# Performance work log

Hardware: AMD Instinct MI355X
Metric: run time of the kernel (lower is better)

Reference implementation:

```python
import jax, jax.numpy as jnp
import numpy as np

N_NODES = 50000
N_EDGES = 800000
IN_DIM = 128
HID = 128
OUT_DIM = 128
N_LAYERS = 6
NUM_GRAPHS = 128


def setup_inputs() -> dict:
    key = jax.random.key(0)
    ks = jax.random.split(key, 16)
    s = 0.05
    inp = {
        "x": jax.random.normal(ks[0], (N_NODES, IN_DIM), jnp.float32),
        "edge_index": jax.random.randint(ks[1], (2, N_EDGES), 0, N_NODES, jnp.int64 if jax.config.jax_enable_x64 else jnp.int32).astype(jnp.int32),
        "batch": jnp.sort(jax.random.randint(ks[2], (N_NODES,), 0, NUM_GRAPHS).astype(jnp.int32)),
        # pre linear
        "pre_w": jax.random.normal(ks[3], (IN_DIM, HID), jnp.float32) * s,
        "pre_b": jnp.zeros((HID,), jnp.float32),
        # GIN mlp per layer: Linear(H,H) -> ReLU -> Linear(H,H)
        "conv_w1": jax.random.normal(ks[4], (N_LAYERS, HID, HID), jnp.float32) * s,
        "conv_b1": jnp.zeros((N_LAYERS, HID), jnp.float32),
        "conv_w2": jax.random.normal(ks[5], (N_LAYERS, HID, HID), jnp.float32) * s,
        "conv_b2": jnp.zeros((N_LAYERS, HID), jnp.float32),
        # post MLP: Linear(7H, H) -> ReLU -> Linear(H, out)
        "post_w1": jax.random.normal(ks[6], (HID * (N_LAYERS + 1), HID), jnp.float32) * s,
        "post_b1": jnp.zeros((HID,), jnp.float32),
        "post_w2": jax.random.normal(ks[7], (HID, OUT_DIM), jnp.float32) * s,
        "post_b2": jnp.zeros((OUT_DIM,), jnp.float32),
    }
    return inp


def reference(x, edge_index, batch, pre_w, pre_b, conv_w1, conv_b1, conv_w2, conv_b2,
              post_w1, post_b1, post_w2, post_b2):
    src, dst = edge_index[0], edge_index[1]
    # pre linear
    h = x @ pre_w + pre_b  # [N, H]
    emb_list = [h]
    xres = h
    for i in range(N_LAYERS):
        # GINConv (eps=0): agg_j x_j over in-edges, then (1+eps)*x + agg -> MLP
        msg = h[src]  # [E, H] gather
        agg = jax.ops.segment_sum(msg, dst, num_segments=N_NODES)  # scatter-add
        z = h + agg
        z = jax.nn.relu(z @ conv_w1[i] + conv_b1[i]) @ conv_w2[i] + conv_b2[i]
        if i & 1:
            z = z + xres
            xres = z
        h = jax.nn.relu(z)
        emb_list.append(h)
    emb = jnp.concatenate(emb_list, axis=1)  # [N, (L+1)*H]
    # global add pool over graphs
    pooled = jax.ops.segment_sum(emb, batch, num_segments=NUM_GRAPHS)  # [G, (L+1)*H]
    out = jax.nn.relu(pooled @ post_w1 + post_b1) @ post_w2 + post_b2  # [G, OUT]
    return out
```

## Files before the change

### kernel.cpp

```cpp
#include <hip/hip_runtime.h>
#include <hip/hip_bf16.h>

#define HID 128

using bf16x8 = __attribute__((ext_vector_type(8))) short;
using f32x4  = __attribute__((ext_vector_type(4))) float;

__device__ inline float bf2f(unsigned int u16) {
    union { float f; unsigned int i; } v; v.i = u16 << 16; return v.f;
}
__device__ inline unsigned short f2bf(float f) {
    __hip_bfloat16 h = __float2bfloat16(f);
    return *reinterpret_cast<unsigned short*>(&h);
}


__global__ void zero_i32(int* __restrict__ p, int n) {
    int i = blockIdx.x * blockDim.x + threadIdx.x;
    if (i < n) p[i] = 0;
}

__global__ void count_deg(const int* __restrict__ dst, int* __restrict__ deg, int E) {
    int e = blockIdx.x * blockDim.x + threadIdx.x;
    if (e < E) atomicAdd(&deg[dst[e]], 1);
}

__global__ __launch_bounds__(256) void block_sums(const int* __restrict__ deg,
                                                  int* __restrict__ bsum, int n) {
    __shared__ int red[256];
    int t = threadIdx.x;
    int i = blockIdx.x * 256 + t;
    red[t] = (i < n) ? deg[i] : 0;
    __syncthreads();
    for (int off = 128; off > 0; off >>= 1) {
        if (t < off) red[t] += red[t + off];
        __syncthreads();
    }
    if (t == 0) bsum[blockIdx.x] = red[0];
}

__global__ __launch_bounds__(1024) void scan_bsums(const int* __restrict__ bsum,
                                                   int* __restrict__ bstart, int nb) {
    __shared__ int s[1024];
    int t = threadIdx.x;
    s[t] = (t < nb) ? bsum[t] : 0;
    __syncthreads();
    for (int off = 1; off < 1024; off <<= 1) {
        int v = (t >= off) ? s[t - off] : 0;
        __syncthreads();
        s[t] += v;
        __syncthreads();
    }
    if (t < nb) bstart[t] = (t == 0) ? 0 : s[t - 1];
}

__global__ __launch_bounds__(256) void scan_within(const int* __restrict__ deg,
                                                   const int* __restrict__ bstart,
                                                   int* __restrict__ row_ptr,
                                                   int* __restrict__ pos, int n) {
    __shared__ int s[256];
    int b = blockIdx.x, t = threadIdx.x;
    int i = b * 256 + t;
    int v = (i < n) ? deg[i] : 0;
    s[t] = v;
    __syncthreads();
    for (int off = 1; off < 256; off <<= 1) {
        int u = (t >= off) ? s[t - off] : 0;
        __syncthreads();
        s[t] += u;
        __syncthreads();
    }
    if (i < n) {
        int excl = bstart[b] + s[t] - v;
        row_ptr[i] = excl;
        pos[i] = excl;
        if (i == n - 1) row_ptr[n] = bstart[b] + s[t];
    }
}

__global__ void fill_csr(const int* __restrict__ src, const int* __restrict__ dst,
                         int* __restrict__ pos, int* __restrict__ csr_src, int E) {
    int e = blockIdx.x * blockDim.x + threadIdx.x;
    if (e < E) {
        int p = atomicAdd(&pos[dst[e]], 1);
        csr_src[p] = src[e];
    }
}

__global__ void graph_starts(const int* __restrict__ batch, int* __restrict__ gstart,
                             int n, int G) {
    int g = blockIdx.x * blockDim.x + threadIdx.x;
    if (g > G) return;
    int lo = 0, hi = n;
    while (lo < hi) { int m = (lo + hi) >> 1; if (batch[m] < g) lo = m + 1; else hi = m; }
    gstart[g] = lo;
}


__global__ void f32_to_bf16_vec(const float* __restrict__ in,
                                unsigned short* __restrict__ out, int n8) {
    int i = blockIdx.x * blockDim.x + threadIdx.x;
    if (i >= n8) return;
    const float4* in4 = (const float4*)in;
    float4 a = in4[i * 2], b = in4[i * 2 + 1];
    uint4 o;
    o.x = f2bf(a.x) | ((unsigned)f2bf(a.y) << 16);
    o.y = f2bf(a.z) | ((unsigned)f2bf(a.w) << 16);
    o.z = f2bf(b.x) | ((unsigned)f2bf(b.y) << 16);
    o.w = f2bf(b.z) | ((unsigned)f2bf(b.w) << 16);
    ((uint4*)out)[i] = o;
}

__global__ void transpose_kc(const float* __restrict__ W, unsigned short* __restrict__ Wt,
                             int K, int C, int total) {
    int tid = blockIdx.x * blockDim.x + threadIdx.x;
    if (tid >= total) return;
    int kc = K * C;
    int mat = tid / kc;
    int rem = tid - mat * kc;
    int c = rem / K;
    int k = rem - c * K;
    Wt[tid] = f2bf(W[(size_t)mat * kc + (size_t)k * C + c]);
}

template <bool ODD>
__global__ __launch_bounds__(256) void fused_layer(const unsigned short* __restrict__ hprev,
                                                   const int* __restrict__ row_ptr,
                                                   const int* __restrict__ csr_src,
                                                   const unsigned short* __restrict__ Wt1,
                                                   const float* __restrict__ b1,
                                                   const unsigned short* __restrict__ Wt2,
                                                   const float* __restrict__ b2,
                                                   unsigned short* __restrict__ xres,
                                                   unsigned short* __restrict__ hnext,
                                                   unsigned short* __restrict__ emb_slice,
                                                   int out_stride, int N) {
    __shared__ __align__(16) char zt[16 * 256];
    __shared__ __align__(16) char tt[16 * 256];
    int t = threadIdx.x;
    int rowbase = blockIdx.x * 16;

    {
        int nl = t >> 4;
        int sub = (t >> 3) & 1;
        int lane8 = t & 7;
        int node = rowbase + nl;
        const uint4* h4 = (const uint4*)hprev;
        float sa0=0,sa1=0,sa2=0,sa3=0,sa4=0,sa5=0,sa6=0,sa7=0;
        float sb0=0,sb1=0,sb2=0,sb3=0,sb4=0,sb5=0,sb6=0,sb7=0;
        if (node < N) {
            if (sub == 0) {
                size_t base = (size_t)node * 16;
                uint4 u0 = h4[base + lane8];
                uint4 u1 = h4[base + lane8 + 8];
                sa0 = bf2f(u0.x & 0xffff); sa1 = bf2f(u0.x >> 16);
                sa2 = bf2f(u0.y & 0xffff); sa3 = bf2f(u0.y >> 16);
                sa4 = bf2f(u0.z & 0xffff); sa5 = bf2f(u0.z >> 16);
                sa6 = bf2f(u0.w & 0xffff); sa7 = bf2f(u0.w >> 16);
                sb0 = bf2f(u1.x & 0xffff); sb1 = bf2f(u1.x >> 16);
                sb2 = bf2f(u1.y & 0xffff); sb3 = bf2f(u1.y >> 16);
                sb4 = bf2f(u1.z & 0xffff); sb5 = bf2f(u1.z >> 16);
                sb6 = bf2f(u1.w & 0xffff); sb7 = bf2f(u1.w >> 16);
            }
            int e0 = row_ptr[node], e1 = row_ptr[node + 1];
            int e = e0 + sub;
#define ACC_ROW(v0, v1)                                                   \
            sa0 += bf2f(v0.x & 0xffff); sa1 += bf2f(v0.x >> 16);          \
            sa2 += bf2f(v0.y & 0xffff); sa3 += bf2f(v0.y >> 16);          \
            sa4 += bf2f(v0.z & 0xffff); sa5 += bf2f(v0.z >> 16);          \
            sa6 += bf2f(v0.w & 0xffff); sa7 += bf2f(v0.w >> 16);          \
            sb0 += bf2f(v1.x & 0xffff); sb1 += bf2f(v1.x >> 16);          \
            sb2 += bf2f(v1.y & 0xffff); sb3 += bf2f(v1.y >> 16);          \
            sb4 += bf2f(v1.z & 0xffff); sb5 += bf2f(v1.z >> 16);          \
            sb6 += bf2f(v1.w & 0xffff); sb7 += bf2f(v1.w >> 16);
            for (; e + 6 < e1; e += 8) {
                size_t p0 = (size_t)csr_src[e] * 16;
                size_t p1 = (size_t)csr_src[e + 2] * 16;
                size_t p2 = (size_t)csr_src[e + 4] * 16;
                size_t p3 = (size_t)csr_src[e + 6] * 16;
                uint4 a0 = h4[p0 + lane8], a1 = h4[p0 + lane8 + 8];
                uint4 c0 = h4[p1 + lane8], c1 = h4[p1 + lane8 + 8];
                uint4 d0 = h4[p2 + lane8], d1 = h4[p2 + lane8 + 8];
                uint4 f0 = h4[p3 + lane8], f1 = h4[p3 + lane8 + 8];
                ACC_ROW(a0, a1)
                ACC_ROW(c0, c1)
                ACC_ROW(d0, d1)
                ACC_ROW(f0, f1)
            }
            for (; e < e1; e += 2) {
                size_t p0 = (size_t)csr_src[e] * 16;
                uint4 a0 = h4[p0 + lane8], a1 = h4[p0 + lane8 + 8];
                ACC_ROW(a0, a1)
            }
#undef ACC_ROW
        }
        sa0 += __shfl_xor(sa0, 8); sa1 += __shfl_xor(sa1, 8);
        sa2 += __shfl_xor(sa2, 8); sa3 += __shfl_xor(sa3, 8);
        sa4 += __shfl_xor(sa4, 8); sa5 += __shfl_xor(sa5, 8);
        sa6 += __shfl_xor(sa6, 8); sa7 += __shfl_xor(sa7, 8);
        sb0 += __shfl_xor(sb0, 8); sb1 += __shfl_xor(sb1, 8);
        sb2 += __shfl_xor(sb2, 8); sb3 += __shfl_xor(sb3, 8);
        sb4 += __shfl_xor(sb4, 8); sb5 += __shfl_xor(sb5, 8);
        sb6 += __shfl_xor(sb6, 8); sb7 += __shfl_xor(sb7, 8);
        uint4 o;
        if (sub == 0) {
            o.x = f2bf(sa0) | ((unsigned)f2bf(sa1) << 16);
            o.y = f2bf(sa2) | ((unsigned)f2bf(sa3) << 16);
            o.z = f2bf(sa4) | ((unsigned)f2bf(sa5) << 16);
            o.w = f2bf(sa6) | ((unsigned)f2bf(sa7) << 16);
        } else {
            o.x = f2bf(sb0) | ((unsigned)f2bf(sb1) << 16);
            o.y = f2bf(sb2) | ((unsigned)f2bf(sb3) << 16);
            o.z = f2bf(sb4) | ((unsigned)f2bf(sb5) << 16);
            o.w = f2bf(sb6) | ((unsigned)f2bf(sb7) << 16);
        }
        int chunk = lane8 + sub * 8;
        *(uint4*)(zt + nl * 256 + ((chunk * 16) ^ ((nl & 7) << 4))) = o;
    }
    __syncthreads();

    int wave = t >> 6, lane = t & 63, l15 = lane & 15, l4 = lane >> 4;
    int colbase = wave * 32;

    f32x4 acc[2];
#pragma unroll
    for (int ct = 0; ct < 2; ct++) acc[ct] = (f32x4){0.f, 0.f, 0.f, 0.f};

#pragma unroll
    for (int kk = 0; kk < 4; kk++) {
        int k0 = kk * 32 + l4 * 8;
        bf16x8 a0 = *(const bf16x8*)(zt + l15 * 256 + ((k0 * 2) ^ ((l15 & 7) << 4)));
#pragma unroll
        for (int ct = 0; ct < 2; ct++) {
            bf16x8 b = *(const bf16x8*)&Wt1[(size_t)(colbase + ct * 16 + l15) * HID + k0];
            acc[ct] = __builtin_amdgcn_mfma_f32_16x16x32_bf16(a0, b, acc[ct], 0, 0, 0);
        }
    }

#pragma unroll
    for (int ct = 0; ct < 2; ct++) {
        int col = colbase + ct * 16 + l15;
        float bc = b1[col];
#pragma unroll
        for (int j = 0; j < 4; j++) {
            int r = l4 * 4 + j;
            float v = fmaxf(acc[ct][j] + bc, 0.f);
            *(unsigned short*)(tt + r * 256 + ((col * 2) ^ ((r & 7) << 4))) = f2bf(v);
        }
    }
    __syncthreads();

#pragma unroll
    for (int ct = 0; ct < 2; ct++) acc[ct] = (f32x4){0.f, 0.f, 0.f, 0.f};
#pragma unroll
    for (int kk = 0; kk < 4; kk++) {
        int k0 = kk * 32 + l4 * 8;
        bf16x8 a0 = *(const bf16x8*)(tt + l15 * 256 + ((k0 * 2) ^ ((l15 & 7) << 4)));
#pragma unroll
        for (int ct = 0; ct < 2; ct++) {
            bf16x8 b = *(const bf16x8*)&Wt2[(size_t)(colbase + ct * 16 + l15) * HID + k0];
            acc[ct] = __builtin_amdgcn_mfma_f32_16x16x32_bf16(a0, b, acc[ct], 0, 0, 0);
        }
    }

#pragma unroll
    for (int ct = 0; ct < 2; ct++) {
        int col = colbase + ct * 16 + l15;
        float bc = b2[col];
#pragma unroll
        for (int j = 0; j < 4; j++) {
            int r = l4 * 4 + j;
            int rg = rowbase + r;
            if (rg < N) {
                float v = acc[ct][j] + bc;
                if (ODD) {
                    v += bf2f(xres[(size_t)rg * HID + col]);
                    xres[(size_t)rg * HID + col] = f2bf(v);
                }
                unsigned short hv = f2bf(fmaxf(v, 0.f));
                hnext[(size_t)rg * HID + col] = hv;
                emb_slice[(size_t)rg * out_stride + col] = hv;
            }
        }
    }
}

__global__ __launch_bounds__(256) void linear_pre(const unsigned short* __restrict__ in,
                                                  const unsigned short* __restrict__ Wt,
                                                  const float* __restrict__ bias,
                                                  unsigned short* __restrict__ emb0,
                                                  int out_stride,
                                                  unsigned short* __restrict__ hcompact,
                                                  unsigned short* __restrict__ pre_out, int M) {
    int tid = threadIdx.x;
    int wave = tid >> 6, lane = tid & 63;
    int l15 = lane & 15, l4 = lane >> 4;
    int rowbase = blockIdx.x * 64 + wave * 16;
    f32x4 acc[8];
#pragma unroll
    for (int ct = 0; ct < 8; ct++) acc[ct] = (f32x4){0.f, 0.f, 0.f, 0.f};
    int r0 = min(rowbase + l15, M - 1);
#pragma unroll
    for (int kk = 0; kk < 4; kk++) {
        int k0 = kk * 32 + l4 * 8;
        bf16x8 a0 = *(const bf16x8*)&in[(size_t)r0 * HID + k0];
#pragma unroll
        for (int ct = 0; ct < 8; ct++) {
            bf16x8 b = *(const bf16x8*)&Wt[(size_t)(ct * 16 + l15) * HID + k0];
            acc[ct] = __builtin_amdgcn_mfma_f32_16x16x32_bf16(a0, b, acc[ct], 0, 0, 0);
        }
    }
#pragma unroll
    for (int ct = 0; ct < 8; ct++) {
        int col = ct * 16 + l15;
        float bc = bias[col];
#pragma unroll
        for (int j = 0; j < 4; j++) {
            int r = rowbase + l4 * 4 + j;
            if (r < M) {
                float v = acc[ct][j] + bc;
                unsigned short bv = f2bf(v);
                pre_out[(size_t)r * HID + col] = bv;
                hcompact[(size_t)r * HID + col] = bv;
                emb0[(size_t)r * out_stride + col] = bv;
            }
        }
    }
}

__global__ __launch_bounds__(128) void pool_all(const unsigned short* __restrict__ emb,
                                                const int* __restrict__ gstart,
                                                float* __restrict__ part, int EMB) {
    int g = blockIdx.x >> 3, sub = blockIdx.x & 7;
    int t = threadIdx.x;
    if (t >= 112) return;
    const uint4* e4 = (const uint4*)emb;
    int row_u4 = EMB / 8;
    int n0 = gstart[g], n1 = gstart[g + 1];
    float s[8] = {0.f, 0.f, 0.f, 0.f, 0.f, 0.f, 0.f, 0.f};
    for (int n = n0 + sub; n < n1; n += 8) {
        uint4 v = e4[(size_t)n * row_u4 + t];
        s[0] += bf2f(v.x & 0xffff); s[1] += bf2f(v.x >> 16);
        s[2] += bf2f(v.y & 0xffff); s[3] += bf2f(v.y >> 16);
        s[4] += bf2f(v.z & 0xffff); s[5] += bf2f(v.z >> 16);
        s[6] += bf2f(v.w & 0xffff); s[7] += bf2f(v.w >> 16);
    }
    float4* p4 = (float4*)&part[(size_t)blockIdx.x * EMB + t * 8];
    p4[0] = (float4){s[0], s[1], s[2], s[3]};
    p4[1] = (float4){s[4], s[5], s[6], s[7]};
}

__global__ __launch_bounds__(128) void pool_fin(const float* __restrict__ part,
                                                unsigned short* __restrict__ pooled,
                                                int EMB) {
    int idx = blockIdx.x * 128 + threadIdx.x;
    int g = idx / EMB, c = idx - g * EMB;
    float s = 0.f;
#pragma unroll
    for (int sub = 0; sub < 8; sub++)
        s += part[(size_t)(g * 8 + sub) * EMB + c];
    pooled[idx] = f2bf(s);
}

__global__ __launch_bounds__(256) void post_mfma(const unsigned short* __restrict__ pooled,
                                                 const unsigned short* __restrict__ w1t,
                                                 const float* __restrict__ b1,
                                                 const unsigned short* __restrict__ w2t,
                                                 const float* __restrict__ b2,
                                                 float* __restrict__ out, int EMB) {
    __shared__ __align__(16) char lds[128 * 256];
    int t = threadIdx.x;
    int wave = t >> 6, lane = t & 63, l15 = lane & 15, l4 = lane >> 4;
    int wrow = wave * 32;
    f32x4 acc[2][8];
#pragma unroll
    for (int rt = 0; rt < 2; rt++)
#pragma unroll
        for (int ct = 0; ct < 8; ct++) acc[rt][ct] = (f32x4){0.f, 0.f, 0.f, 0.f};
    int r0 = wrow + l15, r1 = r0 + 16;
#pragma unroll 4
    for (int kk = 0; kk < EMB / 32; kk++) {
        int k0 = kk * 32 + l4 * 8;
        bf16x8 a0 = *(const bf16x8*)&pooled[(size_t)r0 * EMB + k0];
        bf16x8 a1 = *(const bf16x8*)&pooled[(size_t)r1 * EMB + k0];
#pragma unroll
        for (int ct = 0; ct < 8; ct++) {
            bf16x8 b = *(const bf16x8*)&w1t[(size_t)(ct * 16 + l15) * EMB + k0];
            acc[0][ct] = __builtin_amdgcn_mfma_f32_16x16x32_bf16(a0, b, acc[0][ct], 0, 0, 0);
            acc[1][ct] = __builtin_amdgcn_mfma_f32_16x16x32_bf16(a1, b, acc[1][ct], 0, 0, 0);
        }
    }
#pragma unroll
    for (int ct = 0; ct < 8; ct++) {
        int col = ct * 16 + l15;
        float bc = b1[col];
#pragma unroll
        for (int rt = 0; rt < 2; rt++)
#pragma unroll
            for (int j = 0; j < 4; j++) {
                int r = wrow + rt * 16 + l4 * 4 + j;
                float v = fmaxf(acc[rt][ct][j] + bc, 0.f);
                *(unsigned short*)(lds + r * 256 + ((col * 2) ^ ((r & 7) << 4))) = f2bf(v);
            }
    }
    __syncthreads();
#pragma unroll
    for (int rt = 0; rt < 2; rt++)
#pragma unroll
        for (int ct = 0; ct < 8; ct++) acc[rt][ct] = (f32x4){0.f, 0.f, 0.f, 0.f};
#pragma unroll
    for (int kk = 0; kk < 4; kk++) {
        int k0 = kk * 32 + l4 * 8;
        bf16x8 a0 = *(const bf16x8*)(lds + r0 * 256 + ((k0 * 2) ^ ((r0 & 7) << 4)));
        bf16x8 a1 = *(const bf16x8*)(lds + r1 * 256 + ((k0 * 2) ^ ((r1 & 7) << 4)));
#pragma unroll
        for (int ct = 0; ct < 8; ct++) {
            bf16x8 b = *(const bf16x8*)&w2t[(size_t)(ct * 16 + l15) * HID + k0];
            acc[0][ct] = __builtin_amdgcn_mfma_f32_16x16x32_bf16(a0, b, acc[0][ct], 0, 0, 0);
            acc[1][ct] = __builtin_amdgcn_mfma_f32_16x16x32_bf16(a1, b, acc[1][ct], 0, 0, 0);
        }
    }
#pragma unroll
    for (int ct = 0; ct < 8; ct++) {
        int col = ct * 16 + l15;
        float bc = b2[col];
#pragma unroll
        for (int rt = 0; rt < 2; rt++)
#pragma unroll
            for (int j = 0; j < 4; j++) {
                int r = wrow + rt * 16 + l4 * 4 + j;
                out[(size_t)r * HID + col] = acc[rt][ct][j] + bc;
            }
    }
}


extern "C" void kernel_launch(void* const* d_in, const int* in_sizes, int n_in,
                              void* d_out, int out_size, void* d_ws, size_t ws_size,
                              hipStream_t stream) {
    const float* x       = (const float*)d_in[0];
    const int* edge_index= (const int*)d_in[1];
    const int* batch     = (const int*)d_in[2];
    const float* pre_w   = (const float*)d_in[3];
    const float* pre_b   = (const float*)d_in[4];
    const float* conv_w1 = (const float*)d_in[5];
    const float* conv_b1 = (const float*)d_in[6];
    const float* conv_w2 = (const float*)d_in[7];
    const float* conv_b2 = (const float*)d_in[8];
    const float* post_w1 = (const float*)d_in[9];
    const float* post_b1 = (const float*)d_in[10];
    const float* post_w2 = (const float*)d_in[11];
    const float* post_b2 = (const float*)d_in[12];
    float* outp = (float*)d_out;

    int N = in_sizes[0] / HID;
    int E = in_sizes[1] / 2;
    int L = in_sizes[5] / (HID * HID);
    int G = out_size / HID;
    int EMB = (L + 1) * HID;

    const int* src = edge_index;
    const int* dst = edge_index + E;

    char* w = (char*)d_ws;
    auto alloc = [&](size_t bytes) -> char* {
        char* p = w;
        w += (bytes + 255) & ~(size_t)255;
        return p;
    };
    unsigned short* emb   = (unsigned short*)alloc((size_t)N * EMB * 2);
    unsigned short* hA    = (unsigned short*)alloc((size_t)N * HID * 2);
    unsigned short* hB    = (unsigned short*)alloc((size_t)N * HID * 2);
    unsigned short* x_bf  = (unsigned short*)alloc((size_t)N * HID * 2);
    unsigned short* xres  = (unsigned short*)alloc((size_t)N * HID * 2);
    float* part   = (float*)alloc((size_t)G * 8 * EMB * 4);
    unsigned short* pooled = (unsigned short*)alloc((size_t)G * EMB * 2);
    unsigned short* Wt_pre = (unsigned short*)alloc((size_t)HID * HID * 2);
    unsigned short* Wt_c1  = (unsigned short*)alloc((size_t)L * HID * HID * 2);
    unsigned short* Wt_c2  = (unsigned short*)alloc((size_t)L * HID * HID * 2);
    unsigned short* w1t    = (unsigned short*)alloc((size_t)EMB * HID * 2);
    unsigned short* w2t    = (unsigned short*)alloc((size_t)HID * HID * 2);
    int* deg      = (int*)alloc((size_t)(N + 1) * 4);
    int* row_ptr  = (int*)alloc((size_t)(N + 1) * 4);
    int* pos      = (int*)alloc((size_t)(N + 1) * 4);
    int* bsum     = (int*)alloc((size_t)1024 * 4);
    int* bstart   = (int*)alloc((size_t)1024 * 4);
    int* csr_src  = (int*)alloc((size_t)E * 4);
    int* gstart   = (int*)alloc((size_t)(G + 1) * 4);
    (void)ws_size; (void)n_in;

    int eb = (E + 255) / 256;
    int nb = (N + 255) / 256;

    zero_i32<<<nb, 256, 0, stream>>>(deg, N);
    count_deg<<<eb, 256, 0, stream>>>(dst, deg, E);
    block_sums<<<nb, 256, 0, stream>>>(deg, bsum, N);
    scan_bsums<<<1, 1024, 0, stream>>>(bsum, bstart, nb);
    scan_within<<<nb, 256, 0, stream>>>(deg, bstart, row_ptr, pos, N);
    fill_csr<<<eb, 256, 0, stream>>>(src, dst, pos, csr_src, E);
    graph_starts<<<1, 256, 0, stream>>>(batch, gstart, N, G);

    f32_to_bf16_vec<<<(N * HID / 8 + 255) / 256, 256, 0, stream>>>(x, x_bf, N * HID / 8);
    transpose_kc<<<(HID * HID + 255) / 256, 256, 0, stream>>>(pre_w, Wt_pre, HID, HID, HID * HID);
    transpose_kc<<<(L * HID * HID + 255) / 256, 256, 0, stream>>>(conv_w1, Wt_c1, HID, HID, L * HID * HID);
    transpose_kc<<<(L * HID * HID + 255) / 256, 256, 0, stream>>>(conv_w2, Wt_c2, HID, HID, L * HID * HID);
    transpose_kc<<<(EMB * HID + 255) / 256, 256, 0, stream>>>(post_w1, w1t, EMB, HID, EMB * HID);
    transpose_kc<<<(HID * HID + 255) / 256, 256, 0, stream>>>(post_w2, w2t, HID, HID, HID * HID);

    int gb64 = (N + 63) / 64;
    int gb16 = (N + 15) / 16;

    linear_pre<<<gb64, 256, 0, stream>>>(x_bf, Wt_pre, pre_b, emb, EMB, hA, xres, N);

    unsigned short* hcur = hA;
    unsigned short* hnxt = hB;
    for (int i = 0; i < L; i++) {
        unsigned short* slice_out = emb + (size_t)(i + 1) * HID;
        if (i & 1) {
            fused_layer<true><<<gb16, 256, 0, stream>>>(
                hcur, row_ptr, csr_src,
                Wt_c1 + (size_t)i * HID * HID, conv_b1 + i * HID,
                Wt_c2 + (size_t)i * HID * HID, conv_b2 + i * HID,
                xres, hnxt, slice_out, EMB, N);
        } else {
            fused_layer<false><<<gb16, 256, 0, stream>>>(
                hcur, row_ptr, csr_src,
                Wt_c1 + (size_t)i * HID * HID, conv_b1 + i * HID,
                Wt_c2 + (size_t)i * HID * HID, conv_b2 + i * HID,
                xres, hnxt, slice_out, EMB, N);
        }
        unsigned short* tmp = hcur; hcur = hnxt; hnxt = tmp;
    }

    pool_all<<<G * 8, 128, 0, stream>>>(emb, gstart, part, EMB);
    pool_fin<<<(G * EMB) / 128, 128, 0, stream>>>(part, pooled, EMB);
    post_mfma<<<1, 256, 0, stream>>>(pooled, w1t, post_b1, w2t, post_b2, outp, EMB);
}
```

Before: 580.7 us.

## Gather from emb slices directly and widen fused layer to 512 threads

The separate compact h ping-pong buffers are removed. Each fused layer now gathers neighbour rows straight from the previous slice of the strided emb buffer and writes its output only once, into emb. This drops one N×128 bf16 store per layer and one per pre-linear. The block grows to 512 threads: four lanes-groups split each node's edge list and are combined with an extra shuffle stage, and the MFMA column tiles are spread over 8 waves. In exchange, gathered rows are strided across a larger buffer, and each wave issues half as many MFMAs per weight load.

```diff
diff --git a/kernel.cpp b/kernel.cpp
--- a/kernel.cpp
+++ b/kernel.cpp
@@ -124,7 +124,8 @@
 }
 
 template <bool ODD>
-__global__ __launch_bounds__(256) void fused_layer(const unsigned short* __restrict__ hprev,
+__global__ __launch_bounds__(512) void fused_layer(const unsigned short* __restrict__ emb,
+                                                   int slice_u4, int row_u4,
                                                    const int* __restrict__ row_ptr,
                                                    const int* __restrict__ csr_src,
                                                    const unsigned short* __restrict__ Wt1,
@@ -132,8 +133,7 @@
                                                    const unsigned short* __restrict__ Wt2,
                                                    const float* __restrict__ b2,
                                                    unsigned short* __restrict__ xres,
-                                                   unsigned short* __restrict__ hnext,
-                                                   unsigned short* __restrict__ emb_slice,
+                                                   unsigned short* __restrict__ h_out,
                                                    int out_stride, int N) {
     __shared__ __align__(16) char zt[16 * 256];
     __shared__ __align__(16) char tt[16 * 256];
@@ -141,16 +141,16 @@
     int rowbase = blockIdx.x * 16;
 
     {
-        int nl = t >> 4;
-        int sub = (t >> 3) & 1;
+        int nl = t >> 5;
+        int sub = (t >> 3) & 3;
         int lane8 = t & 7;
         int node = rowbase + nl;
-        const uint4* h4 = (const uint4*)hprev;
+        const uint4* h4 = (const uint4*)emb;
         float sa0=0,sa1=0,sa2=0,sa3=0,sa4=0,sa5=0,sa6=0,sa7=0;
         float sb0=0,sb1=0,sb2=0,sb3=0,sb4=0,sb5=0,sb6=0,sb7=0;
         if (node < N) {
             if (sub == 0) {
-                size_t base = (size_t)node * 16;
+                size_t base = (size_t)node * row_u4 + slice_u4;
                 uint4 u0 = h4[base + lane8];
                 uint4 u1 = h4[base + lane8 + 8];
                 sa0 = bf2f(u0.x & 0xffff); sa1 = bf2f(u0.x >> 16);
@@ -173,113 +173,104 @@
             sb2 += bf2f(v1.y & 0xffff); sb3 += bf2f(v1.y >> 16);          \
             sb4 += bf2f(v1.z & 0xffff); sb5 += bf2f(v1.z >> 16);          \
             sb6 += bf2f(v1.w & 0xffff); sb7 += bf2f(v1.w >> 16);
-            for (; e + 6 < e1; e += 8) {
-                size_t p0 = (size_t)csr_src[e] * 16;
-                size_t p1 = (size_t)csr_src[e + 2] * 16;
-                size_t p2 = (size_t)csr_src[e + 4] * 16;
-                size_t p3 = (size_t)csr_src[e + 6] * 16;
+            for (; e + 4 < e1; e += 8) {
+                size_t p0 = (size_t)csr_src[e] * row_u4 + slice_u4;
+                size_t p1 = (size_t)csr_src[e + 4] * row_u4 + slice_u4;
                 uint4 a0 = h4[p0 + lane8], a1 = h4[p0 + lane8 + 8];
                 uint4 c0 = h4[p1 + lane8], c1 = h4[p1 + lane8 + 8];
-                uint4 d0 = h4[p2 + lane8], d1 = h4[p2 + lane8 + 8];
-                uint4 f0 = h4[p3 + lane8], f1 = h4[p3 + lane8 + 8];
                 ACC_ROW(a0, a1)
                 ACC_ROW(c0, c1)
-                ACC_ROW(d0, d1)
-                ACC_ROW(f0, f1)
-            }
-            for (; e < e1; e += 2) {
-                size_t p0 = (size_t)csr_src[e] * 16;
+            }
+            if (e < e1) {
+                size_t p0 = (size_t)csr_src[e] * row_u4 + slice_u4;
                 uint4 a0 = h4[p0 + lane8], a1 = h4[p0 + lane8 + 8];
                 ACC_ROW(a0, a1)
             }
 #undef ACC_ROW
         }
-        sa0 += __shfl_xor(sa0, 8); sa1 += __shfl_xor(sa1, 8);
-        sa2 += __shfl_xor(sa2, 8); sa3 += __shfl_xor(sa3, 8);
-        sa4 += __shfl_xor(sa4, 8); sa5 += __shfl_xor(sa5, 8);
-        sa6 += __shfl_xor(sa6, 8); sa7 += __shfl_xor(sa7, 8);
-        sb0 += __shfl_xor(sb0, 8); sb1 += __shfl_xor(sb1, 8);
-        sb2 += __shfl_xor(sb2, 8); sb3 += __shfl_xor(sb3, 8);
-        sb4 += __shfl_xor(sb4, 8); sb5 += __shfl_xor(sb5, 8);
-        sb6 += __shfl_xor(sb6, 8); sb7 += __shfl_xor(sb7, 8);
-        uint4 o;
-        if (sub == 0) {
-            o.x = f2bf(sa0) | ((unsigned)f2bf(sa1) << 16);
-            o.y = f2bf(sa2) | ((unsigned)f2bf(sa3) << 16);
-            o.z = f2bf(sa4) | ((unsigned)f2bf(sa5) << 16);
-            o.w = f2bf(sa6) | ((unsigned)f2bf(sa7) << 16);
-        } else {
-            o.x = f2bf(sb0) | ((unsigned)f2bf(sb1) << 16);
-            o.y = f2bf(sb2) | ((unsigned)f2bf(sb3) << 16);
-            o.z = f2bf(sb4) | ((unsigned)f2bf(sb5) << 16);
-            o.w = f2bf(sb6) | ((unsigned)f2bf(sb7) << 16);
-        }
-        int chunk = lane8 + sub * 8;
-        *(uint4*)(zt + nl * 256 + ((chunk * 16) ^ ((nl & 7) << 4))) = o;
+        sa0 += __shfl_xor(sa0, 8);  sa1 += __shfl_xor(sa1, 8);
+        sa2 += __shfl_xor(sa2, 8);  sa3 += __shfl_xor(sa3, 8);
+        sa4 += __shfl_xor(sa4, 8);  sa5 += __shfl_xor(sa5, 8);
+        sa6 += __shfl_xor(sa6, 8);  sa7 += __shfl_xor(sa7, 8);
+        sb0 += __shfl_xor(sb0, 8);  sb1 += __shfl_xor(sb1, 8);
+        sb2 += __shfl_xor(sb2, 8);  sb3 += __shfl_xor(sb3, 8);
+        sb4 += __shfl_xor(sb4, 8);  sb5 += __shfl_xor(sb5, 8);
+        sb6 += __shfl_xor(sb6, 8);  sb7 += __shfl_xor(sb7, 8);
+        sa0 += __shfl_xor(sa0, 16); sa1 += __shfl_xor(sa1, 16);
+        sa2 += __shfl_xor(sa2, 16); sa3 += __shfl_xor(sa3, 16);
+        sa4 += __shfl_xor(sa4, 16); sa5 += __shfl_xor(sa5, 16);
+        sa6 += __shfl_xor(sa6, 16); sa7 += __shfl_xor(sa7, 16);
+        sb0 += __shfl_xor(sb0, 16); sb1 += __shfl_xor(sb1, 16);
+        sb2 += __shfl_xor(sb2, 16); sb3 += __shfl_xor(sb3, 16);
+        sb4 += __shfl_xor(sb4, 16); sb5 += __shfl_xor(sb5, 16);
+        sb6 += __shfl_xor(sb6, 16); sb7 += __shfl_xor(sb7, 16);
+        if (sub < 2) {
+            uint4 o;
+            if (sub == 0) {
+                o.x = f2bf(sa0) | ((unsigned)f2bf(sa1) << 16);
+                o.y = f2bf(sa2) | ((unsigned)f2bf(sa3) << 16);
+                o.z = f2bf(sa4) | ((unsigned)f2bf(sa5) << 16);
+                o.w = f2bf(sa6) | ((unsigned)f2bf(sa7) << 16);
+            } else {
+                o.x = f2bf(sb0) | ((unsigned)f2bf(sb1) << 16);
+                o.y = f2bf(sb2) | ((unsigned)f2bf(sb3) << 16);
+                o.z = f2bf(sb4) | ((unsigned)f2bf(sb5) << 16);
+                o.w = f2bf(sb6) | ((unsigned)f2bf(sb7) << 16);
+            }
+            int chunk = lane8 + sub * 8;
+            *(uint4*)(zt + nl * 256 + ((chunk * 16) ^ ((nl & 7) << 4))) = o;
+        }
     }
     __syncthreads();
 
     int wave = t >> 6, lane = t & 63, l15 = lane & 15, l4 = lane >> 4;
-    int colbase = wave * 32;
-
-    f32x4 acc[2];
-#pragma unroll
-    for (int ct = 0; ct < 2; ct++) acc[ct] = (f32x4){0.f, 0.f, 0.f, 0.f};
+    int colbase = wave * 16;
+
+    f32x4 acc = (f32x4){0.f, 0.f, 0.f, 0.f};
 
 #pragma unroll
     for (int kk = 0; kk < 4; kk++) {
         int k0 = kk * 32 + l4 * 8;
         bf16x8 a0 = *(const bf16x8*)(zt + l15 * 256 + ((k0 * 2) ^ ((l15 & 7) << 4)));
-#pragma unroll
-        for (int ct = 0; ct < 2; ct++) {
-            bf16x8 b = *(const bf16x8*)&Wt1[(size_t)(colbase + ct * 16 + l15) * HID + k0];
-            acc[ct] = __builtin_amdgcn_mfma_f32_16x16x32_bf16(a0, b, acc[ct], 0, 0, 0);
-        }
-    }
-
-#pragma unroll
-    for (int ct = 0; ct < 2; ct++) {
-        int col = colbase + ct * 16 + l15;
+        bf16x8 b = *(const bf16x8*)&Wt1[(size_t)(colbase + l15) * HID + k0];
+        acc = __builtin_amdgcn_mfma_f32_16x16x32_bf16(a0, b, acc, 0, 0, 0);
+    }
+
+    {
+        int col = colbase + l15;
         float bc = b1[col];
 #pragma unroll
         for (int j = 0; j < 4; j++) {
             int r = l4 * 4 + j;
-            float v = fmaxf(acc[ct][j] + bc, 0.f);
+            float v = fmaxf(acc[j] + bc, 0.f);
             *(unsigned short*)(tt + r * 256 + ((col * 2) ^ ((r & 7) << 4))) = f2bf(v);
         }
     }
     __syncthreads();
 
-#pragma unroll
-    for (int ct = 0; ct < 2; ct++) acc[ct] = (f32x4){0.f, 0.f, 0.f, 0.f};
+    acc = (f32x4){0.f, 0.f, 0.f, 0.f};
 #pragma unroll
     for (int kk = 0; kk < 4; kk++) {
         int k0 = kk * 32 + l4 * 8;
         bf16x8 a0 = *(const bf16x8*)(tt + l15 * 256 + ((k0 * 2) ^ ((l15 & 7) << 4)));
-#pragma unroll
-        for (int ct = 0; ct < 2; ct++) {
-            bf16x8 b = *(const bf16x8*)&Wt2[(size_t)(colbase + ct * 16 + l15) * HID + k0];
-            acc[ct] = __builtin_amdgcn_mfma_f32_16x16x32_bf16(a0, b, acc[ct], 0, 0, 0);
-        }
-    }
-
-#pragma unroll
-    for (int ct = 0; ct < 2; ct++) {
-        int col = colbase + ct * 16 + l15;
+        bf16x8 b = *(const bf16x8*)&Wt2[(size_t)(colbase + l15) * HID + k0];
+        acc = __builtin_amdgcn_mfma_f32_16x16x32_bf16(a0, b, acc, 0, 0, 0);
+    }
+
+    {
+        int col = colbase + l15;
         float bc = b2[col];
 #pragma unroll
         for (int j = 0; j < 4; j++) {
             int r = l4 * 4 + j;
             int rg = rowbase + r;
             if (rg < N) {
-                float v = acc[ct][j] + bc;
+                float v = acc[j] + bc;
                 if (ODD) {
                     v += bf2f(xres[(size_t)rg * HID + col]);
                     xres[(size_t)rg * HID + col] = f2bf(v);
                 }
-                unsigned short hv = f2bf(fmaxf(v, 0.f));
-                hnext[(size_t)rg * HID + col] = hv;
-                emb_slice[(size_t)rg * out_stride + col] = hv;
+                h_out[(size_t)rg * out_stride + col] = f2bf(fmaxf(v, 0.f));
             }
         }
     }
@@ -288,9 +279,8 @@
 __global__ __launch_bounds__(256) void linear_pre(const unsigned short* __restrict__ in,
                                                   const unsigned short* __restrict__ Wt,
                                                   const float* __restrict__ bias,
-                                                  unsigned short* __restrict__ emb0,
+                                                  unsigned short* __restrict__ out,
                                                   int out_stride,
-                                                  unsigned short* __restrict__ hcompact,
                                                   unsigned short* __restrict__ pre_out, int M) {
     int tid = threadIdx.x;
     int wave = tid >> 6, lane = tid & 63;
@@ -321,8 +311,7 @@
                 float v = acc[ct][j] + bc;
                 unsigned short bv = f2bf(v);
                 pre_out[(size_t)r * HID + col] = bv;
-                hcompact[(size_t)r * HID + col] = bv;
-                emb0[(size_t)r * out_stride + col] = bv;
+                out[(size_t)r * out_stride + col] = bv;
             }
         }
     }
@@ -469,8 +458,6 @@
         return p;
     };
     unsigned short* emb   = (unsigned short*)alloc((size_t)N * EMB * 2);
-    unsigned short* hA    = (unsigned short*)alloc((size_t)N * HID * 2);
-    unsigned short* hB    = (unsigned short*)alloc((size_t)N * HID * 2);
     unsigned short* x_bf  = (unsigned short*)alloc((size_t)N * HID * 2);
     unsigned short* xres  = (unsigned short*)alloc((size_t)N * HID * 2);
     float* part   = (float*)alloc((size_t)G * 8 * EMB * 4);
@@ -510,26 +497,23 @@
     int gb64 = (N + 63) / 64;
     int gb16 = (N + 15) / 16;
 
-    linear_pre<<<gb64, 256, 0, stream>>>(x_bf, Wt_pre, pre_b, emb, EMB, hA, xres, N);
-
-    unsigned short* hcur = hA;
-    unsigned short* hnxt = hB;
+    linear_pre<<<gb64, 256, 0, stream>>>(x_bf, Wt_pre, pre_b, emb, EMB, xres, N);
+
     for (int i = 0; i < L; i++) {
         unsigned short* slice_out = emb + (size_t)(i + 1) * HID;
         if (i & 1) {
-            fused_layer<true><<<gb16, 256, 0, stream>>>(
-                hcur, row_ptr, csr_src,
+            fused_layer<true><<<gb16, 512, 0, stream>>>(
+                emb, i * 16, EMB / 8, row_ptr, csr_src,
                 Wt_c1 + (size_t)i * HID * HID, conv_b1 + i * HID,
                 Wt_c2 + (size_t)i * HID * HID, conv_b2 + i * HID,
-                xres, hnxt, slice_out, EMB, N);
+                xres, slice_out, EMB, N);
         } else {
-            fused_layer<false><<<gb16, 256, 0, stream>>>(
-                hcur, row_ptr, csr_src,
+            fused_layer<false><<<gb16, 512, 0, stream>>>(
+                emb, i * 16, EMB / 8, row_ptr, csr_src,
                 Wt_c1 + (size_t)i * HID * HID, conv_b1 + i * HID,
                 Wt_c2 + (size_t)i * HID * HID, conv_b2 + i * HID,
-                xres, hnxt, slice_out, EMB, N);
-        }
-        unsigned short* tmp = hcur; hcur = hnxt; hnxt = tmp;
+                xres, slice_out, EMB, N);
+        }
     }
 
     pool_all<<<G * 8, 128, 0, stream>>>(emb, gstart, part, EMB);
```

New measurement: 535.1 us. -7.9%, faster.
